# Kernel tuning notes

Hardware: AMD Instinct MI355X
Metric: run time of the kernel (lower is better)

The kernel has to match this reference:

```python
import jax, jax.numpy as jnp
import numpy as np

B, N, D, E = 4, 8192, 128, 262144


def setup_inputs() -> dict:
    key = jax.random.key(0)
    k_h, k_e, k_w1, k_b1, k_w2, k_b2 = jax.random.split(key, 6)
    h = jax.random.normal(k_h, (B, N, D), dtype=jnp.float32)
    edge_index = jax.random.randint(k_e, (2, E), 0, N, dtype=jnp.int64)
    # edge_mlp: Linear(2D -> D), SiLU, Linear(D -> 1). Kaiming-uniform-ish init scale.
    lim1 = 1.0 / np.sqrt(2 * D)
    lim2 = 1.0 / np.sqrt(D)
    W1 = jax.random.uniform(k_w1, (2 * D, D), minval=-lim1, maxval=lim1, dtype=jnp.float32)
    b1 = jax.random.uniform(k_b1, (D,), minval=-lim1, maxval=lim1, dtype=jnp.float32)
    W2 = jax.random.uniform(k_w2, (D, 1), minval=-lim2, maxval=lim2, dtype=jnp.float32)
    b2 = jax.random.uniform(k_b2, (1,), minval=-lim2, maxval=lim2, dtype=jnp.float32)
    return {"h": h, "edge_index": edge_index, "W1": W1, "b1": b1, "W2": W2, "b2": b2}


def reference(h, edge_index, W1, b1, W2, b2):
    # h: (B, N, D); edge_index: (2, E)
    src, dst = edge_index[0], edge_index[1]
    h_src = h[:, src, :]                                  # (B, E, D) gather
    h_dst = h[:, dst, :]                                  # (B, E, D) gather
    x = jnp.concatenate([h_src, h_dst], axis=-1)          # (B, E, 2D)
    hid = jax.nn.silu(jnp.einsum('bef,fd->bed', x, W1) + b1)  # (B, E, D)
    edge_scores = (jnp.einsum('bed,do->beo', hid, W2) + b2)[..., 0]  # (B, E)
    out = jnp.zeros((B, N, N), dtype=h.dtype)
    out = out.at[:, src, dst].set(edge_scores)            # scatter into dense (B, N, N)
    return out
```

## Files before the change

kernel.cpp:

```cpp
#include <hip/hip_runtime.h>
#include <hip/hip_bf16.h>
#include <stdint.h>

#define B_ 4
#define N_ 8192
#define D_ 128
#define E_ 262144

typedef __bf16 bf16x8 __attribute__((ext_vector_type(8)));
typedef unsigned short u16x8 __attribute__((ext_vector_type(8)));
typedef float f32x4 __attribute__((ext_vector_type(4)));

constexpr int HASH_LOG = 20;
constexpr unsigned HASH_SIZE = 1u << HASH_LOG;
constexpr unsigned HASH_MASK = HASH_SIZE - 1u;
constexpr int BUCKET_CAP = 128;

constexpr size_t OFF_HB     = 0;
constexpr size_t OFF_W1T    = 8388608;
constexpr size_t OFF_HASH   = 8454144;
constexpr size_t OFF_SCORES = 16842752;
constexpr size_t OFF_CNT    = 21037056;
constexpr size_t OFF_BUCKET = 21069824;

__device__ __forceinline__ unsigned short f2bf(float f) {
  union { float f; unsigned u; } v; v.f = f;
  unsigned r = v.u + 0x7fffu + ((v.u >> 16) & 1u);
  return (unsigned short)(r >> 16);
}

__global__ void cast_h_k(const float* __restrict__ h, unsigned short* __restrict__ o) {
  int i = blockIdx.x * blockDim.x + threadIdx.x;
  float4 v = reinterpret_cast<const float4*>(h)[i];
  ushort4 r;
  r.x = f2bf(v.x); r.y = f2bf(v.y); r.z = f2bf(v.z); r.w = f2bf(v.w);
  reinterpret_cast<ushort4*>(o)[i] = r;
}

__global__ void tw1_k(const float* __restrict__ W1, unsigned short* __restrict__ o) {
  int i = blockIdx.x * blockDim.x + threadIdx.x;
  int d = i >> 8, k = i & 255;
  o[i] = f2bf(W1[k * 128 + d]);
}

__global__ void hash_insert_k(const int* __restrict__ ei,
                              unsigned long long* __restrict__ tab) {
  int e = blockIdx.x * blockDim.x + threadIdx.x;
  unsigned s = (unsigned)ei[e];
  unsigned d = (unsigned)ei[E_ + e];
  unsigned key = s * (unsigned)N_ + d;
  unsigned long long pack = (((unsigned long long)(key + 1u)) << 32) | (unsigned long long)(unsigned)e;
  unsigned slot = (key * 2654435761u) & HASH_MASK;
  for (;;) {
    unsigned long long cur = tab[slot];
    if (cur == 0ull) {
      unsigned long long prev = atomicCAS(&tab[slot], 0ull, pack);
      if (prev == 0ull) return;
      cur = prev;
    }
    if ((cur >> 32) == (unsigned long long)(key + 1u)) {
      atomicMax(&tab[slot], pack);
      return;
    }
    slot = (slot + 1u) & HASH_MASK;
  }
}

__global__ void winner_place_k(const int* __restrict__ ei,
                               const unsigned long long* __restrict__ tab,
                               int* __restrict__ cnt, int* __restrict__ bucket) {
  int e = blockIdx.x * blockDim.x + threadIdx.x;
  unsigned s = (unsigned)ei[e];
  unsigned d = (unsigned)ei[E_ + e];
  unsigned key = s * (unsigned)N_ + d;
  unsigned slot = (key * 2654435761u) & HASH_MASK;
  for (;;) {
    unsigned long long cur = tab[slot];
    if ((cur >> 32) == (unsigned long long)(key + 1u)) {
      if ((unsigned)(cur & 0xffffffffull) == (unsigned)e) {
        int pos = atomicAdd(&cnt[s], 1);
        if (pos < BUCKET_CAP) bucket[s * BUCKET_CAP + pos] = e;
      }
      return;
    }
    slot = (slot + 1u) & HASH_MASK;
  }
}

__global__ __launch_bounds__(512, 4) void edge_mlp_k(
    const int* __restrict__ ei,
    const unsigned short* __restrict__ hb,
    const unsigned short* __restrict__ w1t,
    const float* __restrict__ b1,
    const float* __restrict__ w2,
    const float* __restrict__ b2,
    float4* __restrict__ scores) {
  __shared__ char lds[65536];
  const int tid  = threadIdx.x;
  const int lane = tid & 63;
  const int wid  = tid >> 6;
  const int l15  = lane & 15;
  const int lg   = lane >> 4;

  {
    const uint4* g = reinterpret_cast<const uint4*>(w1t);
    #pragma unroll
    for (int it = 0; it < 8; ++it) {
      int i = it * 512 + tid;
      uint4 v = g[i];
      int byte = i * 16;
      int dd = byte >> 9;
      int within = byte & 511;
      *reinterpret_cast<uint4*>(&lds[dd * 512 + (within ^ ((dd & 7) << 4))]) = v;
    }
  }

  const int e0 = blockIdx.x * 64;

  unsigned offS[2], offD[2];
  #pragma unroll
  for (int m = 0; m < 2; ++m) {
    int row = wid * 32 + m * 16 + l15;
    int e = e0 + (row >> 2);
    int b = row & 3;
    offS[m] = ((unsigned)b * N_ + (unsigned)ei[e]) * D_;
    offD[m] = ((unsigned)b * N_ + (unsigned)ei[E_ + e]) * D_;
  }

  __syncthreads();

  f32x4 acc[2][8];
  #pragma unroll
  for (int m = 0; m < 2; ++m)
    #pragma unroll
    for (int n = 0; n < 8; ++n)
      acc[m][n] = (f32x4){0.f, 0.f, 0.f, 0.f};

  const int kg = 8 * lg;

  #pragma unroll
  for (int ks = 0; ks < 8; ++ks) {
    bf16x8 a[2];
    const int kin = (ks & 3) * 32 + kg;
    #pragma unroll
    for (int m = 0; m < 2; ++m) {
      unsigned off = (ks < 4 ? offS[m] : offD[m]) + (unsigned)kin;
      u16x8 u = *reinterpret_cast<const u16x8*>(hb + off);
      a[m] = __builtin_bit_cast(bf16x8, u);
    }
    const int kb = ks * 64 + 16 * lg;
    #pragma unroll
    for (int n = 0; n < 8; ++n) {
      int dd = n * 16 + l15;
      uint4 v = *reinterpret_cast<const uint4*>(&lds[dd * 512 + (kb ^ ((dd & 7) << 4))]);
      bf16x8 bfr = __builtin_bit_cast(bf16x8, v);
      acc[0][n] = __builtin_amdgcn_mfma_f32_16x16x32_bf16(a[0], bfr, acc[0][n], 0, 0, 0);
      acc[1][n] = __builtin_amdgcn_mfma_f32_16x16x32_bf16(a[1], bfr, acc[1][n], 0, 0, 0);
    }
  }

  float b1v[8], w2v[8];
  #pragma unroll
  for (int n = 0; n < 8; ++n) {
    int col = n * 16 + l15;
    b1v[n] = b1[col];
    w2v[n] = w2[col];
  }
  float sc[2][4];
  #pragma unroll
  for (int m = 0; m < 2; ++m)
    #pragma unroll
    for (int i = 0; i < 4; ++i) sc[m][i] = 0.f;
  #pragma unroll
  for (int n = 0; n < 8; ++n)
    #pragma unroll
    for (int m = 0; m < 2; ++m)
      #pragma unroll
      for (int i = 0; i < 4; ++i) {
        float v = acc[m][n][i] + b1v[n];
        float sv = v / (1.f + __expf(-v));
        sc[m][i] += sv * w2v[n];
      }
  #pragma unroll
  for (int m = 0; m < 2; ++m)
    #pragma unroll
    for (int i = 0; i < 4; ++i) {
      float v = sc[m][i];
      v += __shfl_xor(v, 1, 64);
      v += __shfl_xor(v, 2, 64);
      v += __shfl_xor(v, 4, 64);
      v += __shfl_xor(v, 8, 64);
      sc[m][i] = v;
    }
  const float b2v = b2[0];
  if (l15 == 0) {
    #pragma unroll
    for (int m = 0; m < 2; ++m) {
      int base = wid * 32 + m * 16 + 4 * lg;
      scores[e0 + (base >> 2)] =
          make_float4(sc[m][0] + b2v, sc[m][1] + b2v, sc[m][2] + b2v, sc[m][3] + b2v);
    }
  }
}

__global__ __launch_bounds__(256, 8) void out_writer_k(
    const int* __restrict__ ei,
    const int* __restrict__ cnt,
    const int* __restrict__ bucket,
    const float4* __restrict__ scores,
    float* __restrict__ out) {
  __shared__ int   dst_l[BUCKET_CAP];
  __shared__ float sc_l[BUCKET_CAP][4];
  const int t = threadIdx.x;
  const int src = blockIdx.x;
  int n = cnt[src];
  n = n < BUCKET_CAP ? n : BUCKET_CAP;
  if (t < n) {
    int e = bucket[src * BUCKET_CAP + t];
    dst_l[t] = ei[E_ + e];
    float4 s = scores[e];
    sc_l[t][0] = s.x; sc_l[t][1] = s.y; sc_l[t][2] = s.z; sc_l[t][3] = s.w;
  }
  __syncthreads();

  const float4 z = {0.f, 0.f, 0.f, 0.f};
  const size_t rowbase = (size_t)src * N_;
  #pragma unroll
  for (int b = 0; b < 4; ++b) {
    float* rp = out + (size_t)b * ((size_t)N_ * N_) + rowbase;
    float4* po = reinterpret_cast<float4*>(rp);
    #pragma unroll
    for (int k = 0; k < 8; ++k)
      po[t + 256 * k] = z;
    for (int j = 0; j < n; ++j) {
      int dst = dst_l[j];
      if (((dst >> 2) & 255) == t)
        rp[dst] = sc_l[j][b];
    }
  }
}

extern "C" void kernel_launch(void* const* d_in, const int* in_sizes, int n_in,
                              void* d_out, int out_size, void* d_ws, size_t ws_size,
                              hipStream_t stream) {
  const float* h  = (const float*)d_in[0];
  const int*   ei = (const int*)d_in[1];
  const float* W1 = (const float*)d_in[2];
  const float* b1 = (const float*)d_in[3];
  const float* W2 = (const float*)d_in[4];
  const float* b2 = (const float*)d_in[5];
  float* out = (float*)d_out;
  char*  ws  = (char*)d_ws;

  unsigned short*     hb     = (unsigned short*)(ws + OFF_HB);
  unsigned short*     w1t    = (unsigned short*)(ws + OFF_W1T);
  unsigned long long* tab    = (unsigned long long*)(ws + OFF_HASH);
  float4*             scores = (float4*)(ws + OFF_SCORES);
  int*                cnt    = (int*)(ws + OFF_CNT);
  int*                bucket = (int*)(ws + OFF_BUCKET);

  (void)hipMemsetAsync(tab, 0, (size_t)HASH_SIZE * 8, stream);
  (void)hipMemsetAsync(cnt, 0, (size_t)N_ * 4, stream);

  cast_h_k<<<4096, 256, 0, stream>>>(h, hb);
  tw1_k<<<128, 256, 0, stream>>>(W1, w1t);
  hash_insert_k<<<E_ / 256, 256, 0, stream>>>(ei, tab);
  winner_place_k<<<E_ / 256, 256, 0, stream>>>(ei, tab, cnt, bucket);
  edge_mlp_k<<<E_ / 64, 512, 0, stream>>>(ei, hb, w1t, b1, W2, b2, scores);
  out_writer_k<<<N_, 256, 0, stream>>>(ei, cnt, bucket, scores, out);
}
```

Baseline: 1.286 ms.

## Replace global hash dedup with per-source bucket dedup and source-sorted MLP order

Drops the global hash-table pass and its 8 MB memset for duplicate (src,dst) edges. Edges are now bucketed by source, and duplicates are resolved inside the output-writer block with an O(n^2) check in LDS, keeping the largest edge index. A prefix scan builds a source-sorted edge order that the persistent-tile MLP kernel uses to improve locality when gathering h rows. The output writer now builds a byte index map and streams rows with nontemporal vector stores instead of zeroing the row and then scattering. The cost is extra small kernels, including a single-block scan and a serial order build, and edges past the 128-per-source cap are silently dropped.

```diff
diff --git a/kernel.cpp b/kernel.cpp
--- a/kernel.cpp
+++ b/kernel.cpp
@@ -11,17 +11,17 @@
 typedef unsigned short u16x8 __attribute__((ext_vector_type(8)));
 typedef float f32x4 __attribute__((ext_vector_type(4)));
 
-constexpr int HASH_LOG = 20;
-constexpr unsigned HASH_SIZE = 1u << HASH_LOG;
-constexpr unsigned HASH_MASK = HASH_SIZE - 1u;
 constexpr int BUCKET_CAP = 128;
+constexpr int TILES = 8;
+constexpr int GRID_MLP = E_ / (64 * TILES);
 
 constexpr size_t OFF_HB     = 0;
 constexpr size_t OFF_W1T    = 8388608;
-constexpr size_t OFF_HASH   = 8454144;
-constexpr size_t OFF_SCORES = 16842752;
-constexpr size_t OFF_CNT    = 21037056;
-constexpr size_t OFF_BUCKET = 21069824;
+constexpr size_t OFF_SCORES = 8454144;
+constexpr size_t OFF_CNT    = 12648448;
+constexpr size_t OFF_BASE   = 12681216;
+constexpr size_t OFF_BUCKET = 12713984;
+constexpr size_t OFF_ORDER  = 16908288;
 
 __device__ __forceinline__ unsigned short f2bf(float f) {
   union { float f; unsigned u; } v; v.f = f;
@@ -43,58 +43,56 @@
   o[i] = f2bf(W1[k * 128 + d]);
 }
 
-__global__ void hash_insert_k(const int* __restrict__ ei,
-                              unsigned long long* __restrict__ tab) {
+__global__ void place_k(const int* __restrict__ ei,
+                        int* __restrict__ cnt, int* __restrict__ bucket) {
   int e = blockIdx.x * blockDim.x + threadIdx.x;
-  unsigned s = (unsigned)ei[e];
-  unsigned d = (unsigned)ei[E_ + e];
-  unsigned key = s * (unsigned)N_ + d;
-  unsigned long long pack = (((unsigned long long)(key + 1u)) << 32) | (unsigned long long)(unsigned)e;
-  unsigned slot = (key * 2654435761u) & HASH_MASK;
-  for (;;) {
-    unsigned long long cur = tab[slot];
-    if (cur == 0ull) {
-      unsigned long long prev = atomicCAS(&tab[slot], 0ull, pack);
-      if (prev == 0ull) return;
-      cur = prev;
-    }
-    if ((cur >> 32) == (unsigned long long)(key + 1u)) {
-      atomicMax(&tab[slot], pack);
-      return;
-    }
-    slot = (slot + 1u) & HASH_MASK;
-  }
-}
-
-__global__ void winner_place_k(const int* __restrict__ ei,
-                               const unsigned long long* __restrict__ tab,
-                               int* __restrict__ cnt, int* __restrict__ bucket) {
-  int e = blockIdx.x * blockDim.x + threadIdx.x;
-  unsigned s = (unsigned)ei[e];
-  unsigned d = (unsigned)ei[E_ + e];
-  unsigned key = s * (unsigned)N_ + d;
-  unsigned slot = (key * 2654435761u) & HASH_MASK;
-  for (;;) {
-    unsigned long long cur = tab[slot];
-    if ((cur >> 32) == (unsigned long long)(key + 1u)) {
-      if ((unsigned)(cur & 0xffffffffull) == (unsigned)e) {
-        int pos = atomicAdd(&cnt[s], 1);
-        if (pos < BUCKET_CAP) bucket[s * BUCKET_CAP + pos] = e;
-      }
-      return;
-    }
-    slot = (slot + 1u) & HASH_MASK;
-  }
+  int s = ei[e];
+  int pos = atomicAdd(&cnt[s], 1);
+  if (pos < BUCKET_CAP) bucket[s * BUCKET_CAP + pos] = e;
+}
+
+__global__ void prefix_k(const int* __restrict__ cnt, int* __restrict__ base) {
+  __shared__ int sc[256];
+  const int t = threadIdx.x;
+  int c[32];
+  int local = 0;
+  #pragma unroll
+  for (int j = 0; j < 32; ++j) {
+    int v = cnt[t * 32 + j];
+    v = v < BUCKET_CAP ? v : BUCKET_CAP;
+    c[j] = v; local += v;
+  }
+  sc[t] = local;
+  __syncthreads();
+  #pragma unroll
+  for (int off = 1; off < 256; off <<= 1) {
+    int v = (t >= off) ? sc[t - off] : 0;
+    __syncthreads();
+    sc[t] += v;
+    __syncthreads();
+  }
+  int run = sc[t] - local;
+  #pragma unroll
+  for (int j = 0; j < 32; ++j) { base[t * 32 + j] = run; run += c[j]; }
+}
+
+__global__ void order_build_k(const int* __restrict__ cnt, const int* __restrict__ base,
+                              const int* __restrict__ bucket, int* __restrict__ order) {
+  int s = blockIdx.x * blockDim.x + threadIdx.x;
+  int n = cnt[s]; n = n < BUCKET_CAP ? n : BUCKET_CAP;
+  int b0 = base[s];
+  for (int j = 0; j < n; ++j) order[b0 + j] = bucket[s * BUCKET_CAP + j];
 }
 
 __global__ __launch_bounds__(512, 4) void edge_mlp_k(
     const int* __restrict__ ei,
+    const int* __restrict__ order,
     const unsigned short* __restrict__ hb,
     const unsigned short* __restrict__ w1t,
     const float* __restrict__ b1,
     const float* __restrict__ w2,
     const float* __restrict__ b2,
-    float4* __restrict__ scores) {
+    f32x4* __restrict__ scores) {
   __shared__ char lds[65536];
   const int tid  = threadIdx.x;
   const int lane = tid & 63;
@@ -114,50 +112,7 @@
       *reinterpret_cast<uint4*>(&lds[dd * 512 + (within ^ ((dd & 7) << 4))]) = v;
     }
   }
-
-  const int e0 = blockIdx.x * 64;
-
-  unsigned offS[2], offD[2];
-  #pragma unroll
-  for (int m = 0; m < 2; ++m) {
-    int row = wid * 32 + m * 16 + l15;
-    int e = e0 + (row >> 2);
-    int b = row & 3;
-    offS[m] = ((unsigned)b * N_ + (unsigned)ei[e]) * D_;
-    offD[m] = ((unsigned)b * N_ + (unsigned)ei[E_ + e]) * D_;
-  }
-
-  __syncthreads();
-
-  f32x4 acc[2][8];
-  #pragma unroll
-  for (int m = 0; m < 2; ++m)
-    #pragma unroll
-    for (int n = 0; n < 8; ++n)
-      acc[m][n] = (f32x4){0.f, 0.f, 0.f, 0.f};
-
-  const int kg = 8 * lg;
-
-  #pragma unroll
-  for (int ks = 0; ks < 8; ++ks) {
-    bf16x8 a[2];
-    const int kin = (ks & 3) * 32 + kg;
-    #pragma unroll
-    for (int m = 0; m < 2; ++m) {
-      unsigned off = (ks < 4 ? offS[m] : offD[m]) + (unsigned)kin;
-      u16x8 u = *reinterpret_cast<const u16x8*>(hb + off);
-      a[m] = __builtin_bit_cast(bf16x8, u);
-    }
-    const int kb = ks * 64 + 16 * lg;
-    #pragma unroll
-    for (int n = 0; n < 8; ++n) {
-      int dd = n * 16 + l15;
-      uint4 v = *reinterpret_cast<const uint4*>(&lds[dd * 512 + (kb ^ ((dd & 7) << 4))]);
-      bf16x8 bfr = __builtin_bit_cast(bf16x8, v);
-      acc[0][n] = __builtin_amdgcn_mfma_f32_16x16x32_bf16(a[0], bfr, acc[0][n], 0, 0, 0);
-      acc[1][n] = __builtin_amdgcn_mfma_f32_16x16x32_bf16(a[1], bfr, acc[1][n], 0, 0, 0);
-    }
-  }
+  __syncthreads();
 
   float b1v[8], w2v[8];
   #pragma unroll
@@ -166,39 +121,84 @@
     b1v[n] = b1[col];
     w2v[n] = w2[col];
   }
-  float sc[2][4];
-  #pragma unroll
-  for (int m = 0; m < 2; ++m)
-    #pragma unroll
-    for (int i = 0; i < 4; ++i) sc[m][i] = 0.f;
-  #pragma unroll
-  for (int n = 0; n < 8; ++n)
+  const float b2v = b2[0];
+  const int kg = 8 * lg;
+
+  #pragma unroll 1
+  for (int tile = 0; tile < TILES; ++tile) {
+    const int t0 = (blockIdx.x * TILES + tile) * 64;
+
+    unsigned offS[2], offD[2];
+    #pragma unroll
+    for (int m = 0; m < 2; ++m) {
+      int row = wid * 32 + m * 16 + l15;
+      int e = order[t0 + (row >> 2)];
+      int b = row & 3;
+      offS[m] = ((unsigned)b * N_ + (unsigned)ei[e]) * D_;
+      offD[m] = ((unsigned)b * N_ + (unsigned)ei[E_ + e]) * D_;
+    }
+
+    f32x4 acc[2][8];
     #pragma unroll
     for (int m = 0; m < 2; ++m)
       #pragma unroll
+      for (int n = 0; n < 8; ++n)
+        acc[m][n] = (f32x4){0.f, 0.f, 0.f, 0.f};
+
+    #pragma unroll
+    for (int ks = 0; ks < 8; ++ks) {
+      bf16x8 a[2];
+      const int kin = (ks & 3) * 32 + kg;
+      #pragma unroll
+      for (int m = 0; m < 2; ++m) {
+        unsigned off = (ks < 4 ? offS[m] : offD[m]) + (unsigned)kin;
+        u16x8 u = *reinterpret_cast<const u16x8*>(hb + off);
+        a[m] = __builtin_bit_cast(bf16x8, u);
+      }
+      const int kb = ks * 64 + 16 * lg;
+      #pragma unroll
+      for (int n = 0; n < 8; ++n) {
+        int dd = n * 16 + l15;
+        uint4 v = *reinterpret_cast<const uint4*>(&lds[dd * 512 + (kb ^ ((dd & 7) << 4))]);
+        bf16x8 bfr = __builtin_bit_cast(bf16x8, v);
+        acc[0][n] = __builtin_amdgcn_mfma_f32_16x16x32_bf16(a[0], bfr, acc[0][n], 0, 0, 0);
+        acc[1][n] = __builtin_amdgcn_mfma_f32_16x16x32_bf16(a[1], bfr, acc[1][n], 0, 0, 0);
+      }
+    }
+
+    float sc[2][4];
+    #pragma unroll
+    for (int m = 0; m < 2; ++m)
+      #pragma unroll
+      for (int i = 0; i < 4; ++i) sc[m][i] = 0.f;
+    #pragma unroll
+    for (int n = 0; n < 8; ++n)
+      #pragma unroll
+      for (int m = 0; m < 2; ++m)
+        #pragma unroll
+        for (int i = 0; i < 4; ++i) {
+          float v = acc[m][n][i] + b1v[n];
+          float sv = v / (1.f + __expf(-v));
+          sc[m][i] += sv * w2v[n];
+        }
+    #pragma unroll
+    for (int m = 0; m < 2; ++m)
+      #pragma unroll
       for (int i = 0; i < 4; ++i) {
-        float v = acc[m][n][i] + b1v[n];
-        float sv = v / (1.f + __expf(-v));
-        sc[m][i] += sv * w2v[n];
-      }
-  #pragma unroll
-  for (int m = 0; m < 2; ++m)
-    #pragma unroll
-    for (int i = 0; i < 4; ++i) {
-      float v = sc[m][i];
-      v += __shfl_xor(v, 1, 64);
-      v += __shfl_xor(v, 2, 64);
-      v += __shfl_xor(v, 4, 64);
-      v += __shfl_xor(v, 8, 64);
-      sc[m][i] = v;
-    }
-  const float b2v = b2[0];
-  if (l15 == 0) {
-    #pragma unroll
-    for (int m = 0; m < 2; ++m) {
-      int base = wid * 32 + m * 16 + 4 * lg;
-      scores[e0 + (base >> 2)] =
-          make_float4(sc[m][0] + b2v, sc[m][1] + b2v, sc[m][2] + b2v, sc[m][3] + b2v);
+        float v = sc[m][i];
+        v += __shfl_xor(v, 1, 64);
+        v += __shfl_xor(v, 2, 64);
+        v += __shfl_xor(v, 4, 64);
+        v += __shfl_xor(v, 8, 64);
+        sc[m][i] = v;
+      }
+    if (l15 == 0) {
+      #pragma unroll
+      for (int m = 0; m < 2; ++m) {
+        int base_row = wid * 32 + m * 16 + 4 * lg;
+        int e_w = order[t0 + (base_row >> 2)];
+        scores[e_w] = (f32x4){sc[m][0] + b2v, sc[m][1] + b2v, sc[m][2] + b2v, sc[m][3] + b2v};
+      }
     }
   }
 }
@@ -207,35 +207,52 @@
     const int* __restrict__ ei,
     const int* __restrict__ cnt,
     const int* __restrict__ bucket,
-    const float4* __restrict__ scores,
+    const f32x4* __restrict__ scores,
     float* __restrict__ out) {
-  __shared__ int   dst_l[BUCKET_CAP];
-  __shared__ float sc_l[BUCKET_CAP][4];
+  __shared__ int dst_l[BUCKET_CAP];
+  __shared__ int e_l[BUCKET_CAP];
+  __shared__ float sc4[BUCKET_CAP][4];
+  __shared__ unsigned int idx32[2048];
   const int t = threadIdx.x;
   const int src = blockIdx.x;
   int n = cnt[src];
   n = n < BUCKET_CAP ? n : BUCKET_CAP;
   if (t < n) {
     int e = bucket[src * BUCKET_CAP + t];
+    e_l[t] = e;
     dst_l[t] = ei[E_ + e];
-    float4 s = scores[e];
-    sc_l[t][0] = s.x; sc_l[t][1] = s.y; sc_l[t][2] = s.z; sc_l[t][3] = s.w;
-  }
-  __syncthreads();
-
-  const float4 z = {0.f, 0.f, 0.f, 0.f};
+    f32x4 s = scores[e];
+    sc4[t][0] = s[0]; sc4[t][1] = s[1]; sc4[t][2] = s[2]; sc4[t][3] = s[3];
+  }
+  #pragma unroll
+  for (int k = 0; k < 8; ++k) idx32[t + 256 * k] = 0u;
+  __syncthreads();
+  if (t < n) {
+    int dst = dst_l[t], e = e_l[t];
+    bool win = true;
+    for (int j = 0; j < n; ++j)
+      win = win && !(dst_l[j] == dst && e_l[j] > e);
+    if (win) reinterpret_cast<unsigned char*>(idx32)[dst] = (unsigned char)(t + 1);
+  }
+  __syncthreads();
+
   const size_t rowbase = (size_t)src * N_;
   #pragma unroll
   for (int b = 0; b < 4; ++b) {
-    float* rp = out + (size_t)b * ((size_t)N_ * N_) + rowbase;
-    float4* po = reinterpret_cast<float4*>(rp);
-    #pragma unroll
-    for (int k = 0; k < 8; ++k)
-      po[t + 256 * k] = z;
-    for (int j = 0; j < n; ++j) {
-      int dst = dst_l[j];
-      if (((dst >> 2) & 255) == t)
-        rp[dst] = sc_l[j][b];
+    f32x4* po = reinterpret_cast<f32x4*>(out + (size_t)b * ((size_t)N_ * N_) + rowbase);
+    #pragma unroll
+    for (int k = 0; k < 8; ++k) {
+      int c = t + 256 * k;
+      unsigned m4 = idx32[c];
+      f32x4 v = (f32x4){0.f, 0.f, 0.f, 0.f};
+      if (m4) {
+        #pragma unroll
+        for (int i = 0; i < 4; ++i) {
+          unsigned mj = (m4 >> (8 * i)) & 255u;
+          if (mj) v[i] = sc4[mj - 1][b];
+        }
+      }
+      __builtin_nontemporal_store(v, po + c);
     }
   }
 }
@@ -252,20 +269,22 @@
   float* out = (float*)d_out;
   char*  ws  = (char*)d_ws;
 
-  unsigned short*     hb     = (unsigned short*)(ws + OFF_HB);
-  unsigned short*     w1t    = (unsigned short*)(ws + OFF_W1T);
-  unsigned long long* tab    = (unsigned long long*)(ws + OFF_HASH);
-  float4*             scores = (float4*)(ws + OFF_SCORES);
-  int*                cnt    = (int*)(ws + OFF_CNT);
-  int*                bucket = (int*)(ws + OFF_BUCKET);
-
-  (void)hipMemsetAsync(tab, 0, (size_t)HASH_SIZE * 8, stream);
+  unsigned short* hb     = (unsigned short*)(ws + OFF_HB);
+  unsigned short* w1t    = (unsigned short*)(ws + OFF_W1T);
+  f32x4*          scores = (f32x4*)(ws + OFF_SCORES);
+  int*            cnt    = (int*)(ws + OFF_CNT);
+  int*            base   = (int*)(ws + OFF_BASE);
+  int*            bucket = (int*)(ws + OFF_BUCKET);
+  int*            order  = (int*)(ws + OFF_ORDER);
+
   (void)hipMemsetAsync(cnt, 0, (size_t)N_ * 4, stream);
+  (void)hipMemsetAsync(order, 0, (size_t)E_ * 4, stream);
 
   cast_h_k<<<4096, 256, 0, stream>>>(h, hb);
   tw1_k<<<128, 256, 0, stream>>>(W1, w1t);
-  hash_insert_k<<<E_ / 256, 256, 0, stream>>>(ei, tab);
-  winner_place_k<<<E_ / 256, 256, 0, stream>>>(ei, tab, cnt, bucket);
-  edge_mlp_k<<<E_ / 64, 512, 0, stream>>>(ei, hb, w1t, b1, W2, b2, scores);
+  place_k<<<E_ / 256, 256, 0, stream>>>(ei, cnt, bucket);
+  prefix_k<<<1, 256, 0, stream>>>(cnt, base);
+  order_build_k<<<32, 256, 0, stream>>>(cnt, base, bucket, order);
+  edge_mlp_k<<<GRID_MLP, 512, 0, stream>>>(ei, order, hb, w1t, b1, W2, b2, scores);
   out_writer_k<<<N_, 256, 0, stream>>>(ei, cnt, bucket, scores, out);
 }
```

Measured after the change: 1.658 ms. +28.9%, slower.
